# Kernel tuning notes

Hardware: AMD Instinct MI355X
Metric: run time of the kernel (lower is better)

Reference implementation:

```python
import jax, jax.numpy as jnp
import numpy as np

B = 2048      # env batch (graphs)
A = 8         # agents per graph (fully connected)
N = B * A     # total nodes
DIN = 192     # raw obs dim
HD = 256      # h_dim (base MLP)
MD = 256      # mem_dim (GRU)
GD = 128      # gnn_dim (per-head GATv2 out, concat=False -> head mean)
H = 4         # GAT heads
NA = 20       # n_actions
ED = 3        # edge_dim


def setup_inputs() -> dict:
    key = jax.random.key(0)
    ks = jax.random.split(key, 16)
    # fully-connected directed graph per group of A agents, no self loops
    s, d = np.meshgrid(np.arange(A), np.arange(A), indexing='ij')
    mask = s != d
    s = s[mask]; d = d[mask]                     # [A*(A-1)]
    off = (np.arange(B) * A)[:, None]
    src = (off + s[None, :]).reshape(-1)
    dst = (off + d[None, :]).reshape(-1)
    edge_index = jnp.asarray(np.stack([src, dst]), dtype=jnp.int32)  # [2, E]
    E = src.shape[0]
    p = lambda k, sh: jax.random.normal(ks[k], sh, jnp.float32) * 0.02
    return {
        'inputs': jax.random.normal(ks[0], (N, DIN), jnp.float32),
        'hidden_states': jax.random.normal(ks[1], (N, MD), jnp.float32) * 0.1,
        'edge_index': edge_index,
        'edge_attr': jax.random.uniform(ks[2], (E, ED), jnp.float32),
        # base MLP (2 layers: Linear+ReLU+LayerNorm)
        'W1': p(3, (DIN, HD)), 'b1': jnp.zeros(HD), 'g1': jnp.ones(HD), 'be1': jnp.zeros(HD),
        'W2': p(4, (HD, HD)),  'b2': jnp.zeros(HD), 'g2': jnp.ones(HD), 'be2': jnp.zeros(HD),
        # GRUCell
        'Wih': p(5, (3 * MD, HD)), 'Whh': p(6, (3 * MD, MD)),
        'bih': jnp.zeros(3 * MD), 'bhh': jnp.zeros(3 * MD),
        # GATv2Conv (edge_dim=3, heads=4, concat=False, residual)
        'Wl': p(7, (MD, H * GD)), 'bl': jnp.zeros(H * GD),
        'Wr': p(8, (MD, H * GD)), 'br': jnp.zeros(H * GD),
        'att': p(9, (H, GD)),
        'We': p(10, (ED, H * GD)),
        'Wres': p(11, (MD, GD)),
        'bg': jnp.zeros(GD),
        # head: LayerNorm + Linear
        'lng': jnp.ones(GD), 'lnb': jnp.zeros(GD),
        'Wout': p(12, (GD, NA)), 'bout': jnp.zeros(NA),
    }


def _ln(x, g, b):
    mu = jnp.mean(x, -1, keepdims=True)
    xc = x - mu
    v = jnp.mean(xc * xc, -1, keepdims=True)
    return xc * jax.lax.rsqrt(v + 1e-5) * g + b


def _fwd(inputs, hidden_states, edge_attr, edge_index,
         W1, b1, g1, be1, W2, b2, g2, be2,
         Wih, Whh, bih, bhh,
         Wl, bl, Wr, br, att, We, Wres, bg,
         lng, lnb, Wout, bout):
    src, dst = edge_index[0], edge_index[1]
    # ---- base MLP encode ----
    x = _ln(jax.nn.relu(inputs @ W1 + b1), g1, be1)
    x = _ln(jax.nn.relu(x @ W2 + b2), g2, be2)          # [N, HD]
    # ---- SimpleConv(aggr='mean', combine_root='self_loop') ----
    s = jax.ops.segment_sum(x[src], dst, num_segments=N) + x
    deg = jax.ops.segment_sum(jnp.ones(src.shape[0], x.dtype), dst, num_segments=N) + 1.0
    x = s / deg[:, None]                                 # [N, HD]
    # ---- GRUCell ----
    gi = x @ Wih.T + bih
    gh = hidden_states @ Whh.T + bhh
    ir, iz, inn = jnp.split(gi, 3, -1)
    hr, hz, hn = jnp.split(gh, 3, -1)
    r = jax.nn.sigmoid(ir + hr)
    z = jax.nn.sigmoid(iz + hz)
    n = jnp.tanh(inn + r * hn)
    h = (1.0 - z) * n + z * hidden_states                # [N, MD]
    # ---- GATv2Conv (add self loops, edge_attr fill='mean') ----
    loop = jnp.arange(N, dtype=src.dtype)
    sf = jnp.concatenate([src, loop])
    df = jnp.concatenate([dst, loop])
    ea = jnp.concatenate([edge_attr, jnp.broadcast_to(edge_attr.mean(0), (N, ED))], 0)
    xl = (h @ Wl + bl).reshape(N, H, GD)
    xr = (h @ Wr + br).reshape(N, H, GD)
    m = xl[sf] + xr[df] + (ea @ We).reshape(-1, H, GD)   # [Ef, H, GD]
    m = jnp.where(m > 0, m, 0.2 * m)                     # leaky_relu(0.2)
    logits = jnp.einsum('ehc,hc->eh', m, att)            # [Ef, H]
    mx = jax.ops.segment_max(logits, df, num_segments=N)
    ex = jnp.exp(logits - mx[df])
    den = jax.ops.segment_sum(ex, df, num_segments=N)
    alpha = ex / (den[df] + 1e-16)                       # segment softmax
    out = jax.ops.segment_sum(xl[sf] * alpha[..., None], df, num_segments=N)
    out = out.mean(1) + h @ Wres + bg                    # head mean + residual + bias
    zg = jax.nn.relu(out)                                # [N, GD]
    # ---- action head ----
    q = _ln(zg, lng, lnb) @ Wout + bout                  # [N, NA]
    return q, h


def reference(inputs, hidden_states, edge_index, edge_attr,
              W1, b1, g1, be1, W2, b2, g2, be2,
              Wih, Whh, bih, bhh,
              Wl, bl, Wr, br, att, We, Wres, bg,
              lng, lnb, Wout, bout):
    return _fwd(inputs, hidden_states, edge_attr, edge_index,
                W1, b1, g1, be1, W2, b2, g2, be2,
                Wih, Whh, bih, bhh,
                Wl, bl, Wr, br, att, We, Wres, bg,
                lng, lnb, Wout, bout)
```

## Files before the change

kernel.cpp:

```cpp
#include <hip/hip_runtime.h>
#include <hip/hip_bf16.h>

constexpr int NB  = 2048;
constexpr int AG  = 8;
constexpr int NN  = NB * AG;
constexpr int DIN = 192;
constexpr int HD  = 256;
constexpr int MD  = 256;
constexpr int GD  = 128;
constexpr int NA  = 20;
constexpr int NE  = NB * AG * (AG - 1);

typedef __attribute__((ext_vector_type(8))) short bfrag8;
typedef __attribute__((ext_vector_type(4))) short sfrag4;
typedef __attribute__((ext_vector_type(4))) float f32x4;

#define MFMA16(a, b, c) __builtin_amdgcn_mfma_f32_16x16x32_bf16((a), (b), (c), 0, 0, 0)

__device__ __forceinline__ float bf2f(__hip_bfloat16 x) { return __bfloat162float(x); }
__device__ __forceinline__ __hip_bfloat16 f2bf(float x) { return __float2bfloat16(x); }
__device__ __forceinline__ short f2bs(float x) {
    __hip_bfloat16 b = __float2bfloat16(x);
    return *reinterpret_cast<short*>(&b);
}
__device__ __forceinline__ bfrag8 ldf(const __hip_bfloat16* p) { return *(const bfrag8*)p; }
__device__ __forceinline__ bfrag8 ldf32(const float* p) {
    const f32x4 a = *(const f32x4*)p;
    const f32x4 b = *(const f32x4*)(p + 4);
    bfrag8 r;
    r[0] = f2bs(a[0]); r[1] = f2bs(a[1]); r[2] = f2bs(a[2]); r[3] = f2bs(a[3]);
    r[4] = f2bs(b[0]); r[5] = f2bs(b[1]); r[6] = f2bs(b[2]); r[7] = f2bs(b[3]);
    return r;
}
__device__ __forceinline__ float sigmf(float x) { return 1.f / (1.f + __expf(-x)); }
__device__ __forceinline__ float blo(unsigned u) { return __uint_as_float(u << 16); }
__device__ __forceinline__ float bhi(unsigned u) { return __uint_as_float(u & 0xffff0000u); }

__global__ __launch_bounds__(256) void k_prep(
    const float* __restrict__ W1, const float* __restrict__ W2,
    const float* __restrict__ Wih, const float* __restrict__ Whh,
    const float* __restrict__ Wl, const float* __restrict__ bl,
    const float* __restrict__ Wr, const float* __restrict__ br,
    const float* __restrict__ Wres, const float* __restrict__ Wout,
    const float* __restrict__ ea,
    __hip_bfloat16* __restrict__ W1T, __hip_bfloat16* __restrict__ W2T,
    __hip_bfloat16* __restrict__ WihB, __hip_bfloat16* __restrict__ WhhB,
    __hip_bfloat16* __restrict__ WcatT, float* __restrict__ WoutTf,
    float* __restrict__ bcat, float* __restrict__ ea_partials)
{
    __shared__ float sw[4][3];
    const int tid = threadIdx.x;
    if (blockIdx.x >= 3151) {
        const int b = blockIdx.x - 3151;
        float a0 = 0.f, a1 = 0.f, a2 = 0.f;
#pragma unroll
        for (int k = 0; k < 7; k++) {
            int e = b * 1792 + k * 256 + tid;
            a0 += ea[e * 3 + 0];
            a1 += ea[e * 3 + 1];
            a2 += ea[e * 3 + 2];
        }
#pragma unroll
        for (int off = 1; off < 64; off <<= 1) {
            a0 += __shfl_xor(a0, off); a1 += __shfl_xor(a1, off); a2 += __shfl_xor(a2, off);
        }
        if ((tid & 63) == 0) { sw[tid >> 6][0] = a0; sw[tid >> 6][1] = a1; sw[tid >> 6][2] = a2; }
        __syncthreads();
        if (tid == 0) {
            ea_partials[b * 3 + 0] = sw[0][0] + sw[1][0] + sw[2][0] + sw[3][0];
            ea_partials[b * 3 + 1] = sw[0][1] + sw[1][1] + sw[2][1] + sw[3][1];
            ea_partials[b * 3 + 2] = sw[0][2] + sw[1][2] + sw[2][2] + sw[3][2];
        }
        return;
    }
    int i = blockIdx.x * 256 + tid;
    if (i < 49152) { int o = i / 192, c = i % 192; W1T[i] = f2bf(W1[c * 256 + o]); return; }
    i -= 49152;
    if (i < 65536) { int o = i >> 8, c = i & 255; W2T[i] = f2bf(W2[c * 256 + o]); return; }
    i -= 65536;
    if (i < 196608) { WihB[i] = f2bf(Wih[i]); return; }
    i -= 196608;
    if (i < 196608) { WhhB[i] = f2bf(Whh[i]); return; }
    i -= 196608;
    if (i < 294912) {
        int o = i >> 8, c = i & 255;
        float v;
        if (o < 512)       v = Wl[c * 512 + o];
        else if (o < 1024) v = Wr[c * 512 + (o - 512)];
        else               v = Wres[c * 128 + (o - 1024)];
        WcatT[i] = f2bf(v); return;
    }
    i -= 294912;
    if (i < 2560) { int o = i >> 7, c = i & 127; WoutTf[i] = Wout[c * 20 + o]; return; }
    i -= 2560;
    if (i < 1152) {
        float v = 0.f;
        if (i < 512) v = bl[i]; else if (i < 1024) v = br[i - 512];
        bcat[i] = v;
    }
}

__global__ __launch_bounds__(256) void k_encode(
    const float* __restrict__ in,
    const __hip_bfloat16* __restrict__ W1T,
    const float* __restrict__ b1, const float* __restrict__ g1, const float* __restrict__ be1,
    const __hip_bfloat16* __restrict__ W2T,
    const float* __restrict__ b2, const float* __restrict__ g2, const float* __restrict__ be2,
    __hip_bfloat16* __restrict__ xm)
{
    __shared__ float sf[16][257];
    __shared__ alignas(16) __hip_bfloat16 sb[16][264];
    const int tid = threadIdx.x;
    const int lane = tid & 63, w = tid >> 6;
    const int r = lane & 15, q = lane >> 4;
    const int m0 = blockIdx.x * 16;

    {
        bfrag8 af[6];
        const float* ap = in + (size_t)(m0 + r) * DIN + q * 8;
#pragma unroll
        for (int kb = 0; kb < 6; kb++) af[kb] = ldf32(ap + kb * 32);
#pragma unroll
        for (int i = 0; i < 4; i++) {
            int t = w * 4 + i;
            const __hip_bfloat16* wp = W1T + (size_t)(t * 16 + r) * DIN + q * 8;
            bfrag8 bf[6];
#pragma unroll
            for (int kb = 0; kb < 6; kb++) bf[kb] = ldf(wp + kb * 32);
            f32x4 acc = (f32x4){0.f, 0.f, 0.f, 0.f};
#pragma unroll
            for (int kb = 0; kb < 6; kb++) acc = MFMA16(af[kb], bf[kb], acc);
            int col = t * 16 + r;
            float bias = b1[col];
#pragma unroll
            for (int reg = 0; reg < 4; reg++)
                sf[q * 4 + reg][col] = fmaxf(acc[reg] + bias, 0.f);
        }
    }
    __syncthreads();
    {
        int rowi = tid >> 4, c16 = tid & 15;
        float vals[16]; float s = 0.f, s2 = 0.f;
#pragma unroll
        for (int j = 0; j < 16; j++) { float v = sf[rowi][c16 + 16 * j]; vals[j] = v; s += v; s2 += v * v; }
#pragma unroll
        for (int off = 1; off < 16; off <<= 1) { s += __shfl_xor(s, off); s2 += __shfl_xor(s2, off); }
        float mean = s * (1.f / HD);
        float var = fmaxf(s2 * (1.f / HD) - mean * mean, 0.f);
        float rs = rsqrtf(var + 1e-5f);
#pragma unroll
        for (int j = 0; j < 16; j++) {
            int col = c16 + 16 * j;
            sb[rowi][col] = f2bf((vals[j] - mean) * rs * g1[col] + be1[col]);
        }
    }
    __syncthreads();

    {
        bfrag8 af[8];
        const __hip_bfloat16* ap = &sb[r][0];
#pragma unroll
        for (int kb = 0; kb < 8; kb++) af[kb] = ldf(ap + kb * 32 + q * 8);
        float outv[4][4];
#pragma unroll
        for (int i = 0; i < 4; i++) {
            int t = w * 4 + i;
            const __hip_bfloat16* wp = W2T + (size_t)(t * 16 + r) * HD + q * 8;
            bfrag8 bf[8];
#pragma unroll
            for (int kb = 0; kb < 8; kb++) bf[kb] = ldf(wp + kb * 32);
            f32x4 acc = (f32x4){0.f, 0.f, 0.f, 0.f};
#pragma unroll
            for (int kb = 0; kb < 8; kb++) acc = MFMA16(af[kb], bf[kb], acc);
#pragma unroll
            for (int reg = 0; reg < 4; reg++) outv[i][reg] = acc[reg];
        }
        __syncthreads();
#pragma unroll
        for (int i = 0; i < 4; i++) {
            int col = (w * 4 + i) * 16 + r;
            float bias = b2[col];
#pragma unroll
            for (int reg = 0; reg < 4; reg++)
                sf[q * 4 + reg][col] = fmaxf(outv[i][reg] + bias, 0.f);
        }
    }
    __syncthreads();
    {
        int rowi = tid >> 4, c16 = tid & 15;
        float vals[16]; float s = 0.f, s2 = 0.f;
#pragma unroll
        for (int j = 0; j < 16; j++) { float v = sf[rowi][c16 + 16 * j]; vals[j] = v; s += v; s2 += v * v; }
#pragma unroll
        for (int off = 1; off < 16; off <<= 1) { s += __shfl_xor(s, off); s2 += __shfl_xor(s2, off); }
        float mean = s * (1.f / HD);
        float var = fmaxf(s2 * (1.f / HD) - mean * mean, 0.f);
        float rs = rsqrtf(var + 1e-5f);
#pragma unroll
        for (int j = 0; j < 16; j++) {
            int col = c16 + 16 * j;
            sb[rowi][col] = f2bf((vals[j] - mean) * rs * g2[col] + be2[col]);
        }
    }
    __syncthreads();
    {
        int col = tid;
        float a0 = 0.f, a1 = 0.f;
#pragma unroll
        for (int i = 0; i < 8; i++) { a0 += bf2f(sb[i][col]); a1 += bf2f(sb[8 + i][col]); }
        xm[(size_t)(2 * blockIdx.x) * HD + col] = f2bf(a0 * 0.125f);
        xm[(size_t)(2 * blockIdx.x + 1) * HD + col] = f2bf(a1 * 0.125f);
    }
}

__global__ __launch_bounds__(256, 2) void k_gruG(
    const float* __restrict__ hprev,
    const __hip_bfloat16* __restrict__ WhhB,
    const float* __restrict__ bhh,
    const __hip_bfloat16* __restrict__ xm,
    const __hip_bfloat16* __restrict__ WihB,
    const float* __restrict__ bih,
    float* __restrict__ hout)
{
    __shared__ alignas(16) float sgi[16][200];
    const int tid = threadIdx.x;
    const int lane = tid & 63, w = tid >> 6;
    const int r = lane & 15, q = lane >> 4;
    const int bswz = (blockIdx.x & 7) * 64 + (blockIdx.x >> 3);
    const int m0 = (bswz >> 2) * 128;
    const int cg = (bswz & 3) * 64;

    {
        const int g0 = m0 >> 3;
        bfrag8 axm[8];
        const __hip_bfloat16* ap = xm + (size_t)(g0 + r) * MD + q * 8;
#pragma unroll
        for (int kb = 0; kb < 8; kb++) axm[kb] = ldf(ap + kb * 32);
#pragma unroll
        for (int i = 0; i < 3; i++) {
            const int n = w * 3 + i;
            const int gate = n >> 2, nj = n & 3;
            const int colG = gate * 256 + cg + nj * 16 + r;
            const __hip_bfloat16* wp = WihB + (size_t)colG * MD + q * 8;
            bfrag8 bf[8];
#pragma unroll
            for (int kb = 0; kb < 8; kb++) bf[kb] = ldf(wp + kb * 32);
            f32x4 acg = (f32x4){0.f, 0.f, 0.f, 0.f};
#pragma unroll
            for (int kb = 0; kb < 8; kb++) acg = MFMA16(axm[kb], bf[kb], acg);
            const float bias = bih[colG];
#pragma unroll
            for (int reg = 0; reg < 4; reg++)
                sgi[q * 4 + reg][n * 16 + r] = acg[reg] + bias;
        }
    }

    bfrag8 afr[2][8];
#pragma unroll
    for (int t = 0; t < 2; t++) {
        const float* ap = hprev + (size_t)(m0 + (w * 2 + t) * 16 + r) * MD + q * 8;
#pragma unroll
        for (int kb = 0; kb < 8; kb++) afr[t][kb] = ldf32(ap + kb * 32);
    }
    __syncthreads();

    f32x4 acc[2][12];
#pragma unroll
    for (int t = 0; t < 2; t++)
#pragma unroll
        for (int n = 0; n < 12; n++) acc[t][n] = (f32x4){0.f, 0.f, 0.f, 0.f};

#pragma unroll
    for (int kb = 0; kb < 8; kb++) {
        bfrag8 bfB[12];
#pragma unroll
        for (int g = 0; g < 3; g++)
#pragma unroll
            for (int nj = 0; nj < 4; nj++)
                bfB[g * 4 + nj] = ldf(WhhB + (size_t)(g * 256 + cg + nj * 16 + r) * MD
                                      + kb * 32 + q * 8);
#pragma unroll
        for (int t = 0; t < 2; t++)
#pragma unroll
            for (int n = 0; n < 12; n++)
                acc[t][n] = MFMA16(bfB[n], afr[t][kb], acc[t][n]);
    }

#pragma unroll
    for (int t = 0; t < 2; t++) {
        int node = m0 + (w * 2 + t) * 16 + r;
        int gl = ((w * 2 + t) * 16 + r) >> 3;
#pragma unroll
        for (int nj = 0; nj < 4; nj++) {
            int c = cg + nj * 16 + q * 4;
            int ci = nj * 16 + q * 4;
            f32x4 gR = *(const f32x4*)&sgi[gl][ci];
            f32x4 gZ = *(const f32x4*)&sgi[gl][64 + ci];
            f32x4 gN = *(const f32x4*)&sgi[gl][128 + ci];
            f32x4 bR = *(const f32x4*)&bhh[c];
            f32x4 bZ = *(const f32x4*)&bhh[256 + c];
            f32x4 bN = *(const f32x4*)&bhh[512 + c];
            f32x4 hp = *(const f32x4*)&hprev[(size_t)node * MD + c];
            f32x4 hv;
#pragma unroll
            for (int reg = 0; reg < 4; reg++) {
                float rr = sigmf(gR[reg] + acc[t][0 + nj][reg] + bR[reg]);
                float zz = sigmf(gZ[reg] + acc[t][4 + nj][reg] + bZ[reg]);
                float nn = tanhf(gN[reg] + rr * (acc[t][8 + nj][reg] + bN[reg]));
                hv[reg] = (1.f - zz) * nn + zz * hp[reg];
            }
            *(f32x4*)&hout[(size_t)node * MD + c] = hv;
        }
    }
}

__global__ __launch_bounds__(256, 4) void k_gat(
    const float* __restrict__ h,
    const __hip_bfloat16* __restrict__ WcatT,
    const float* __restrict__ bcat,
    const float* __restrict__ ea,
    const float* __restrict__ ea_partials,
    const float* __restrict__ att,
    const float* __restrict__ We,
    const float* __restrict__ bg,
    const float* __restrict__ lng, const float* __restrict__ lnb,
    const float* __restrict__ WoutTf,
    const float* __restrict__ bout,
    float* __restrict__ qout)
{
    __shared__ alignas(16) char smem_raw[16 * 1160 * 2];
    __shared__ float slog[2][4][8][8];
    __shared__ float smean[4];
    __hip_bfloat16 (*sx)[1160] = (__hip_bfloat16 (*)[1160])smem_raw;
    float (*szg)[136] = (float (*)[136])smem_raw;
    const int tid = threadIdx.x;
    const int lane = tid & 63, w = tid >> 6;
    const int m0 = blockIdx.x * 16;

    if (tid < 3) {
        float s = 0.f;
        for (int i = 0; i < 64; i++) s += ea_partials[i * 3 + tid];
        smean[tid] = s * (1.f / NE);
    }

    const int r = lane & 15, q = lane >> 4;
    const int sL = lane & 7, dL = lane >> 3;
    const int gg = w >> 1;
    float e0 = 0.f, e1 = 0.f, e2 = 0.f;
    if (sL != dL) {
        int eidx = sL * 7 + dL - (dL > sL ? 1 : 0);
        const float* ep = ea + (size_t)((blockIdx.x * 2 + gg) * 56 + eidx) * 3;
        e0 = ep[0]; e1 = ep[1]; e2 = ep[2];
    }

    {
        bfrag8 af[8];
        const float* ap = h + (size_t)(m0 + r) * MD + q * 8;
#pragma unroll
        for (int kb = 0; kb < 8; kb++) af[kb] = ldf32(ap + kb * 32);
#pragma unroll
        for (int i = 0; i < 18; i++) {
            const int t = i * 4 + w;
            const __hip_bfloat16* wp = WcatT + (size_t)(t * 16 + r) * MD + q * 8;
            bfrag8 bf[8];
#pragma unroll
            for (int kb = 0; kb < 8; kb++) bf[kb] = ldf(wp + kb * 32);
            f32x4 acc = (f32x4){0.f, 0.f, 0.f, 0.f};
#pragma unroll
            for (int kb = 0; kb < 8; kb++) acc = MFMA16(af[kb], bf[kb], acc);
            const int col = t * 16 + r;
            const float bias = bcat[col];
#pragma unroll
            for (int reg = 0; reg < 4; reg++)
                sx[q * 4 + reg][col] = f2bf(acc[reg] + bias);
        }
    }
    __syncthreads();
    if (sL == dL) { e0 = smean[0]; e1 = smean[1]; e2 = smean[2]; }

    {
        const __hip_bfloat16* xlrow = &sx[gg * 8 + sL][0];
        const __hip_bfloat16* xrrow = &sx[gg * 8 + dL][512];
#pragma unroll
        for (int t = 0; t < 2; t++) {
            const int hh = (w & 1) * 2 + t;
            const int woff = __builtin_amdgcn_readfirstlane(hh * 128);
            const float* attp = att + woff;
            const float* w0p = We + woff;
            const float* w1p = We + 512 + woff;
            const float* w2p = We + 1024 + woff;
            const __hip_bfloat16* xlp = xlrow + hh * 128;
            const __hip_bfloat16* xrp = xrrow + hh * 128;
            float p0 = 0.f, p1 = 0.f;
#pragma unroll 4
            for (int cb = 0; cb < 16; cb++) {
                const uint4 uxl = *(const uint4*)&xlp[cb * 8];
                const uint4 uxr = *(const uint4*)&xrp[cb * 8];
                const f32x4 a0  = *(const f32x4*)&attp[cb * 8];
                const f32x4 a1  = *(const f32x4*)&attp[cb * 8 + 4];
                const f32x4 w00 = *(const f32x4*)&w0p[cb * 8];
                const f32x4 w01 = *(const f32x4*)&w0p[cb * 8 + 4];
                const f32x4 w10 = *(const f32x4*)&w1p[cb * 8];
                const f32x4 w11 = *(const f32x4*)&w1p[cb * 8 + 4];
                const f32x4 w20 = *(const f32x4*)&w2p[cb * 8];
                const f32x4 w21 = *(const f32x4*)&w2p[cb * 8 + 4];
                float mm;
#define CH1(XL, XR, WA, WB, WC, AT, ACC)                                          \
                mm = fmaf(e2, (WC), fmaf(e1, (WB), fmaf(e0, (WA), (XL)))) + (XR); \
                mm = fmaxf(mm, 0.2f * mm); ACC = fmaf(mm, (AT), ACC);
                CH1(blo(uxl.x), blo(uxr.x), w00[0], w10[0], w20[0], a0[0], p0)
                CH1(bhi(uxl.x), bhi(uxr.x), w00[1], w10[1], w20[1], a0[1], p1)
                CH1(blo(uxl.y), blo(uxr.y), w00[2], w10[2], w20[2], a0[2], p0)
                CH1(bhi(uxl.y), bhi(uxr.y), w00[3], w10[3], w20[3], a0[3], p1)
                CH1(blo(uxl.z), blo(uxr.z), w01[0], w11[0], w21[0], a1[0], p0)
                CH1(bhi(uxl.z), bhi(uxr.z), w01[1], w11[1], w21[1], a1[1], p1)
                CH1(blo(uxl.w), blo(uxr.w), w01[2], w11[2], w21[2], a1[2], p0)
                CH1(bhi(uxl.w), bhi(uxr.w), w01[3], w11[3], w21[3], a1[3], p1)
#undef CH1
            }
            float p = p0 + p1;
            float mx = fmaxf(p, __shfl_xor(p, 1));
            mx = fmaxf(mx, __shfl_xor(mx, 2));
            mx = fmaxf(mx, __shfl_xor(mx, 4));
            float exv = __expf(p - mx);
            float den = exv + __shfl_xor(exv, 1);
            den += __shfl_xor(den, 2);
            den += __shfl_xor(den, 4);
            ((float*)&slog[gg][hh][0][0])[lane] = exv / (den + 1e-16f);
        }
    }
    __syncthreads();

    {
        const int d16 = tid >> 4, cb = (tid & 15) * 8;
        const int ag = d16 >> 3, dd = d16 & 7;
        float out[8] = {0.f, 0.f, 0.f, 0.f, 0.f, 0.f, 0.f, 0.f};
#pragma unroll
        for (int hh = 0; hh < 4; hh++) {
#pragma unroll
            for (int s = 0; s < 8; s++) {
                const float al = slog[ag][hh][dd][s];
                const uint4 u = *(const uint4*)&sx[ag * 8 + s][hh * 128 + cb];
                out[0] = fmaf(al, blo(u.x), out[0]);
                out[1] = fmaf(al, bhi(u.x), out[1]);
                out[2] = fmaf(al, blo(u.y), out[2]);
                out[3] = fmaf(al, bhi(u.y), out[3]);
                out[4] = fmaf(al, blo(u.z), out[4]);
                out[5] = fmaf(al, bhi(u.z), out[5]);
                out[6] = fmaf(al, blo(u.w), out[6]);
                out[7] = fmaf(al, bhi(u.w), out[7]);
            }
        }
        const uint4 ur = *(const uint4*)&sx[d16][1024 + cb];
        const f32x4 bg0 = *(const f32x4*)&bg[cb];
        const f32x4 bg1 = *(const f32x4*)&bg[cb + 4];
        f32x4 ov0, ov1;
        ov0[0] = fmaxf(out[0] * 0.25f + blo(ur.x) + bg0[0], 0.f);
        ov0[1] = fmaxf(out[1] * 0.25f + bhi(ur.x) + bg0[1], 0.f);
        ov0[2] = fmaxf(out[2] * 0.25f + blo(ur.y) + bg0[2], 0.f);
        ov0[3] = fmaxf(out[3] * 0.25f + bhi(ur.y) + bg0[3], 0.f);
        ov1[0] = fmaxf(out[4] * 0.25f + blo(ur.z) + bg1[0], 0.f);
        ov1[1] = fmaxf(out[5] * 0.25f + bhi(ur.z) + bg1[1], 0.f);
        ov1[2] = fmaxf(out[6] * 0.25f + blo(ur.w) + bg1[2], 0.f);
        ov1[3] = fmaxf(out[7] * 0.25f + bhi(ur.w) + bg1[3], 0.f);
        __syncthreads();
        *(f32x4*)&szg[d16][cb]     = ov0;
        *(f32x4*)&szg[d16][cb + 4] = ov1;
    }
    __syncthreads();

    {
        int row = tid >> 4, j = tid & 15;
        float v[8]; float s = 0.f, s2 = 0.f;
#pragma unroll
        for (int cj = 0; cj < 8; cj++) { v[cj] = szg[row][j + 16 * cj]; s += v[cj]; s2 += v[cj] * v[cj]; }
#pragma unroll
        for (int off = 1; off < 16; off <<= 1) { s += __shfl_xor(s, off); s2 += __shfl_xor(s2, off); }
        float mean = s * (1.f / GD);
        float var = fmaxf(s2 * (1.f / GD) - mean * mean, 0.f);
        float rs = rsqrtf(var + 1e-5f);
#pragma unroll
        for (int cj = 0; cj < 8; cj++) {
            int c = j + 16 * cj;
            szg[row][c] = (v[cj] - mean) * rs * lng[c] + lnb[c];
        }
    }
    __syncthreads();

    {
        int row = tid >> 4, j = tid & 15;
        for (int jj = j; jj < NA; jj += 16) {
            float a = bout[jj];
            const float* wo = WoutTf + jj * 128;
#pragma unroll
            for (int c4 = 0; c4 < 32; c4++) {
                f32x4 z = *(const f32x4*)&szg[row][c4 * 4];
                const f32x4 wv = *(const f32x4*)&wo[c4 * 4];
                a = fmaf(z[0], wv[0], a); a = fmaf(z[1], wv[1], a);
                a = fmaf(z[2], wv[2], a); a = fmaf(z[3], wv[3], a);
            }
            qout[(size_t)(m0 + row) * NA + jj] = a;
        }
    }
}

extern "C" void kernel_launch(void* const* d_in, const int* in_sizes, int n_in,
                              void* d_out, int out_size, void* d_ws, size_t ws_size,
                              hipStream_t stream) {
    const float* inp   = (const float*)d_in[0];
    const float* hid   = (const float*)d_in[1];
    const float* eatt  = (const float*)d_in[3];
    const float* W1    = (const float*)d_in[4];
    const float* b1    = (const float*)d_in[5];
    const float* g1    = (const float*)d_in[6];
    const float* be1   = (const float*)d_in[7];
    const float* W2    = (const float*)d_in[8];
    const float* b2    = (const float*)d_in[9];
    const float* g2    = (const float*)d_in[10];
    const float* be2   = (const float*)d_in[11];
    const float* Wih   = (const float*)d_in[12];
    const float* Whh   = (const float*)d_in[13];
    const float* bih   = (const float*)d_in[14];
    const float* bhh   = (const float*)d_in[15];
    const float* Wl    = (const float*)d_in[16];
    const float* bl    = (const float*)d_in[17];
    const float* Wr    = (const float*)d_in[18];
    const float* br    = (const float*)d_in[19];
    const float* att   = (const float*)d_in[20];
    const float* We    = (const float*)d_in[21];
    const float* Wres  = (const float*)d_in[22];
    const float* bg    = (const float*)d_in[23];
    const float* lng   = (const float*)d_in[24];
    const float* lnb   = (const float*)d_in[25];
    const float* Wout  = (const float*)d_in[26];
    const float* bout  = (const float*)d_in[27];

    float* qout = (float*)d_out;
    float* hout = (float*)d_out + (size_t)NN * NA;

    char* ws = (char*)d_ws;
    float*           ea_partials = (float*)ws;
    __hip_bfloat16*  xm    = (__hip_bfloat16*)(ws + 2048);
    __hip_bfloat16*  W1T   = (__hip_bfloat16*)(ws + 7342080);
    __hip_bfloat16*  W2T   = (__hip_bfloat16*)(ws + 7440384);
    __hip_bfloat16*  WihB  = (__hip_bfloat16*)(ws + 7571456);
    __hip_bfloat16*  WhhB  = (__hip_bfloat16*)(ws + 7964672);
    __hip_bfloat16*  WcatT = (__hip_bfloat16*)(ws + 8357888);
    float*           bcat  = (float*)(ws + 8947712);
    float*           WoutTf= (float*)(ws + 8952320);

    k_prep<<<3215, 256, 0, stream>>>(W1, W2, Wih, Whh, Wl, bl, Wr, br, Wres, Wout, eatt,
                                     W1T, W2T, WihB, WhhB, WcatT, WoutTf, bcat, ea_partials);
    k_encode<<<NN / 16, 256, 0, stream>>>(inp, W1T, b1, g1, be1, W2T, b2, g2, be2, xm);
    k_gruG<<<512, 256, 0, stream>>>(hid, WhhB, bhh, xm, WihB, bih, hout);
    k_gat<<<NB / 2, 256, 0, stream>>>(hout, WcatT, bcat, eatt, ea_partials, att, We, bg,
                                      lng, lnb, WoutTf, bout, qout);
}
```

Measured before the change: 312.6 us.

## Fuse encoder, GRU and GAT into one per-graph-pair kernel

Merges the encoder MLP, the GRU cell and the GATv2/head kernels into a single kernel where each block handles 16 nodes (2 graphs). The pooled encoder output, the GRU input gates and the new hidden state stay in shared memory and never go through global memory, and two kernel launches are removed. The cost is that each block now runs all GEMMs against a 16-row tile. The Wih GEMM does 16-row MFMAs on only 2 useful rows, and Whh is reloaded per 16 nodes instead of per 128, which raises weight traffic and wasted MFMA work.

```diff
diff --git a/kernel.cpp b/kernel.cpp
--- a/kernel.cpp
+++ b/kernel.cpp
@@ -100,222 +100,17 @@
     }
 }
 
-__global__ __launch_bounds__(256) void k_encode(
+__global__ __launch_bounds__(256, 4) void k_fused(
     const float* __restrict__ in,
     const __hip_bfloat16* __restrict__ W1T,
     const float* __restrict__ b1, const float* __restrict__ g1, const float* __restrict__ be1,
     const __hip_bfloat16* __restrict__ W2T,
     const float* __restrict__ b2, const float* __restrict__ g2, const float* __restrict__ be2,
-    __hip_bfloat16* __restrict__ xm)
-{
-    __shared__ float sf[16][257];
-    __shared__ alignas(16) __hip_bfloat16 sb[16][264];
-    const int tid = threadIdx.x;
-    const int lane = tid & 63, w = tid >> 6;
-    const int r = lane & 15, q = lane >> 4;
-    const int m0 = blockIdx.x * 16;
-
-    {
-        bfrag8 af[6];
-        const float* ap = in + (size_t)(m0 + r) * DIN + q * 8;
-#pragma unroll
-        for (int kb = 0; kb < 6; kb++) af[kb] = ldf32(ap + kb * 32);
-#pragma unroll
-        for (int i = 0; i < 4; i++) {
-            int t = w * 4 + i;
-            const __hip_bfloat16* wp = W1T + (size_t)(t * 16 + r) * DIN + q * 8;
-            bfrag8 bf[6];
-#pragma unroll
-            for (int kb = 0; kb < 6; kb++) bf[kb] = ldf(wp + kb * 32);
-            f32x4 acc = (f32x4){0.f, 0.f, 0.f, 0.f};
-#pragma unroll
-            for (int kb = 0; kb < 6; kb++) acc = MFMA16(af[kb], bf[kb], acc);
-            int col = t * 16 + r;
-            float bias = b1[col];
-#pragma unroll
-            for (int reg = 0; reg < 4; reg++)
-                sf[q * 4 + reg][col] = fmaxf(acc[reg] + bias, 0.f);
-        }
-    }
-    __syncthreads();
-    {
-        int rowi = tid >> 4, c16 = tid & 15;
-        float vals[16]; float s = 0.f, s2 = 0.f;
-#pragma unroll
-        for (int j = 0; j < 16; j++) { float v = sf[rowi][c16 + 16 * j]; vals[j] = v; s += v; s2 += v * v; }
-#pragma unroll
-        for (int off = 1; off < 16; off <<= 1) { s += __shfl_xor(s, off); s2 += __shfl_xor(s2, off); }
-        float mean = s * (1.f / HD);
-        float var = fmaxf(s2 * (1.f / HD) - mean * mean, 0.f);
-        float rs = rsqrtf(var + 1e-5f);
-#pragma unroll
-        for (int j = 0; j < 16; j++) {
-            int col = c16 + 16 * j;
-            sb[rowi][col] = f2bf((vals[j] - mean) * rs * g1[col] + be1[col]);
-        }
-    }
-    __syncthreads();
-
-    {
-        bfrag8 af[8];
-        const __hip_bfloat16* ap = &sb[r][0];
-#pragma unroll
-        for (int kb = 0; kb < 8; kb++) af[kb] = ldf(ap + kb * 32 + q * 8);
-        float outv[4][4];
-#pragma unroll
-        for (int i = 0; i < 4; i++) {
-            int t = w * 4 + i;
-            const __hip_bfloat16* wp = W2T + (size_t)(t * 16 + r) * HD + q * 8;
-            bfrag8 bf[8];
-#pragma unroll
-            for (int kb = 0; kb < 8; kb++) bf[kb] = ldf(wp + kb * 32);
-            f32x4 acc = (f32x4){0.f, 0.f, 0.f, 0.f};
-#pragma unroll
-            for (int kb = 0; kb < 8; kb++) acc = MFMA16(af[kb], bf[kb], acc);
-#pragma unroll
-            for (int reg = 0; reg < 4; reg++) outv[i][reg] = acc[reg];
-        }
-        __syncthreads();
-#pragma unroll
-        for (int i = 0; i < 4; i++) {
-            int col = (w * 4 + i) * 16 + r;
-            float bias = b2[col];
-#pragma unroll
-            for (int reg = 0; reg < 4; reg++)
-                sf[q * 4 + reg][col] = fmaxf(outv[i][reg] + bias, 0.f);
-        }
-    }
-    __syncthreads();
-    {
-        int rowi = tid >> 4, c16 = tid & 15;
-        float vals[16]; float s = 0.f, s2 = 0.f;
-#pragma unroll
-        for (int j = 0; j < 16; j++) { float v = sf[rowi][c16 + 16 * j]; vals[j] = v; s += v; s2 += v * v; }
-#pragma unroll
-        for (int off = 1; off < 16; off <<= 1) { s += __shfl_xor(s, off); s2 += __shfl_xor(s2, off); }
-        float mean = s * (1.f / HD);
-        float var = fmaxf(s2 * (1.f / HD) - mean * mean, 0.f);
-        float rs = rsqrtf(var + 1e-5f);
-#pragma unroll
-        for (int j = 0; j < 16; j++) {
-            int col = c16 + 16 * j;
-            sb[rowi][col] = f2bf((vals[j] - mean) * rs * g2[col] + be2[col]);
-        }
-    }
-    __syncthreads();
-    {
-        int col = tid;
-        float a0 = 0.f, a1 = 0.f;
-#pragma unroll
-        for (int i = 0; i < 8; i++) { a0 += bf2f(sb[i][col]); a1 += bf2f(sb[8 + i][col]); }
-        xm[(size_t)(2 * blockIdx.x) * HD + col] = f2bf(a0 * 0.125f);
-        xm[(size_t)(2 * blockIdx.x + 1) * HD + col] = f2bf(a1 * 0.125f);
-    }
-}
-
-__global__ __launch_bounds__(256, 2) void k_gruG(
     const float* __restrict__ hprev,
     const __hip_bfloat16* __restrict__ WhhB,
     const float* __restrict__ bhh,
-    const __hip_bfloat16* __restrict__ xm,
     const __hip_bfloat16* __restrict__ WihB,
     const float* __restrict__ bih,
-    float* __restrict__ hout)
-{
-    __shared__ alignas(16) float sgi[16][200];
-    const int tid = threadIdx.x;
-    const int lane = tid & 63, w = tid >> 6;
-    const int r = lane & 15, q = lane >> 4;
-    const int bswz = (blockIdx.x & 7) * 64 + (blockIdx.x >> 3);
-    const int m0 = (bswz >> 2) * 128;
-    const int cg = (bswz & 3) * 64;
-
-    {
-        const int g0 = m0 >> 3;
-        bfrag8 axm[8];
-        const __hip_bfloat16* ap = xm + (size_t)(g0 + r) * MD + q * 8;
-#pragma unroll
-        for (int kb = 0; kb < 8; kb++) axm[kb] = ldf(ap + kb * 32);
-#pragma unroll
-        for (int i = 0; i < 3; i++) {
-            const int n = w * 3 + i;
-            const int gate = n >> 2, nj = n & 3;
-            const int colG = gate * 256 + cg + nj * 16 + r;
-            const __hip_bfloat16* wp = WihB + (size_t)colG * MD + q * 8;
-            bfrag8 bf[8];
-#pragma unroll
-            for (int kb = 0; kb < 8; kb++) bf[kb] = ldf(wp + kb * 32);
-            f32x4 acg = (f32x4){0.f, 0.f, 0.f, 0.f};
-#pragma unroll
-            for (int kb = 0; kb < 8; kb++) acg = MFMA16(axm[kb], bf[kb], acg);
-            const float bias = bih[colG];
-#pragma unroll
-            for (int reg = 0; reg < 4; reg++)
-                sgi[q * 4 + reg][n * 16 + r] = acg[reg] + bias;
-        }
-    }
-
-    bfrag8 afr[2][8];
-#pragma unroll
-    for (int t = 0; t < 2; t++) {
-        const float* ap = hprev + (size_t)(m0 + (w * 2 + t) * 16 + r) * MD + q * 8;
-#pragma unroll
-        for (int kb = 0; kb < 8; kb++) afr[t][kb] = ldf32(ap + kb * 32);
-    }
-    __syncthreads();
-
-    f32x4 acc[2][12];
-#pragma unroll
-    for (int t = 0; t < 2; t++)
-#pragma unroll
-        for (int n = 0; n < 12; n++) acc[t][n] = (f32x4){0.f, 0.f, 0.f, 0.f};
-
-#pragma unroll
-    for (int kb = 0; kb < 8; kb++) {
-        bfrag8 bfB[12];
-#pragma unroll
-        for (int g = 0; g < 3; g++)
-#pragma unroll
-            for (int nj = 0; nj < 4; nj++)
-                bfB[g * 4 + nj] = ldf(WhhB + (size_t)(g * 256 + cg + nj * 16 + r) * MD
-                                      + kb * 32 + q * 8);
-#pragma unroll
-        for (int t = 0; t < 2; t++)
-#pragma unroll
-            for (int n = 0; n < 12; n++)
-                acc[t][n] = MFMA16(bfB[n], afr[t][kb], acc[t][n]);
-    }
-
-#pragma unroll
-    for (int t = 0; t < 2; t++) {
-        int node = m0 + (w * 2 + t) * 16 + r;
-        int gl = ((w * 2 + t) * 16 + r) >> 3;
-#pragma unroll
-        for (int nj = 0; nj < 4; nj++) {
-            int c = cg + nj * 16 + q * 4;
-            int ci = nj * 16 + q * 4;
-            f32x4 gR = *(const f32x4*)&sgi[gl][ci];
-            f32x4 gZ = *(const f32x4*)&sgi[gl][64 + ci];
-            f32x4 gN = *(const f32x4*)&sgi[gl][128 + ci];
-            f32x4 bR = *(const f32x4*)&bhh[c];
-            f32x4 bZ = *(const f32x4*)&bhh[256 + c];
-            f32x4 bN = *(const f32x4*)&bhh[512 + c];
-            f32x4 hp = *(const f32x4*)&hprev[(size_t)node * MD + c];
-            f32x4 hv;
-#pragma unroll
-            for (int reg = 0; reg < 4; reg++) {
-                float rr = sigmf(gR[reg] + acc[t][0 + nj][reg] + bR[reg]);
-                float zz = sigmf(gZ[reg] + acc[t][4 + nj][reg] + bZ[reg]);
-                float nn = tanhf(gN[reg] + rr * (acc[t][8 + nj][reg] + bN[reg]));
-                hv[reg] = (1.f - zz) * nn + zz * hp[reg];
-            }
-            *(f32x4*)&hout[(size_t)node * MD + c] = hv;
-        }
-    }
-}
-
-__global__ __launch_bounds__(256, 4) void k_gat(
-    const float* __restrict__ h,
     const __hip_bfloat16* __restrict__ WcatT,
     const float* __restrict__ bcat,
     const float* __restrict__ ea,
@@ -326,15 +121,22 @@
     const float* __restrict__ lng, const float* __restrict__ lnb,
     const float* __restrict__ WoutTf,
     const float* __restrict__ bout,
-    float* __restrict__ qout)
+    float* __restrict__ qout,
+    float* __restrict__ hout)
 {
-    __shared__ alignas(16) char smem_raw[16 * 1160 * 2];
+    __shared__ alignas(16) char smem[16 * 1160 * 2];
     __shared__ float slog[2][4][8][8];
     __shared__ float smean[4];
-    __hip_bfloat16 (*sx)[1160] = (__hip_bfloat16 (*)[1160])smem_raw;
-    float (*szg)[136] = (float (*)[136])smem_raw;
+    float          (*sf)[257]  = (float (*)[257])smem;
+    __hip_bfloat16 (*sb)[264]  = (__hip_bfloat16 (*)[264])(smem + 16448);
+    __hip_bfloat16 (*smx)[264] = (__hip_bfloat16 (*)[264])smem;
+    float          (*sgi)[768] = (float (*)[768])(smem + 24896);
+    __hip_bfloat16 (*sx)[1160] = (__hip_bfloat16 (*)[1160])smem;
+    float          (*szg)[136] = (float (*)[136])smem;
+
     const int tid = threadIdx.x;
     const int lane = tid & 63, w = tid >> 6;
+    const int r = lane & 15, q = lane >> 4;
     const int m0 = blockIdx.x * 16;
 
     if (tid < 3) {
@@ -342,8 +144,6 @@
         for (int i = 0; i < 64; i++) s += ea_partials[i * 3 + tid];
         smean[tid] = s * (1.f / NE);
     }
-
-    const int r = lane & 15, q = lane >> 4;
     const int sL = lane & 7, dL = lane >> 3;
     const int gg = w >> 1;
     float e0 = 0.f, e1 = 0.f, e2 = 0.f;
@@ -354,10 +154,181 @@
     }
 
     {
+        bfrag8 af[6];
+        const float* ap = in + (size_t)(m0 + r) * DIN + q * 8;
+#pragma unroll
+        for (int kb = 0; kb < 6; kb++) af[kb] = ldf32(ap + kb * 32);
+#pragma unroll
+        for (int i = 0; i < 4; i++) {
+            int t = w * 4 + i;
+            const __hip_bfloat16* wp = W1T + (size_t)(t * 16 + r) * DIN + q * 8;
+            bfrag8 bf[6];
+#pragma unroll
+            for (int kb = 0; kb < 6; kb++) bf[kb] = ldf(wp + kb * 32);
+            f32x4 acc = (f32x4){0.f, 0.f, 0.f, 0.f};
+#pragma unroll
+            for (int kb = 0; kb < 6; kb++) acc = MFMA16(af[kb], bf[kb], acc);
+            int col = t * 16 + r;
+            float bias = b1[col];
+#pragma unroll
+            for (int reg = 0; reg < 4; reg++)
+                sf[q * 4 + reg][col] = fmaxf(acc[reg] + bias, 0.f);
+        }
+    }
+    __syncthreads();
+    {
+        int rowi = tid >> 4, c16 = tid & 15;
+        float vals[16]; float s = 0.f, s2 = 0.f;
+#pragma unroll
+        for (int j = 0; j < 16; j++) { float v = sf[rowi][c16 + 16 * j]; vals[j] = v; s += v; s2 += v * v; }
+#pragma unroll
+        for (int off = 1; off < 16; off <<= 1) { s += __shfl_xor(s, off); s2 += __shfl_xor(s2, off); }
+        float mean = s * (1.f / HD);
+        float var = fmaxf(s2 * (1.f / HD) - mean * mean, 0.f);
+        float rs = rsqrtf(var + 1e-5f);
+#pragma unroll
+        for (int j = 0; j < 16; j++) {
+            int col = c16 + 16 * j;
+            sb[rowi][col] = f2bf((vals[j] - mean) * rs * g1[col] + be1[col]);
+        }
+    }
+    __syncthreads();
+    {
         bfrag8 af[8];
-        const float* ap = h + (size_t)(m0 + r) * MD + q * 8;
-#pragma unroll
-        for (int kb = 0; kb < 8; kb++) af[kb] = ldf32(ap + kb * 32);
+        const __hip_bfloat16* ap = &sb[r][0];
+#pragma unroll
+        for (int kb = 0; kb < 8; kb++) af[kb] = ldf(ap + kb * 32 + q * 8);
+        float outv[4][4];
+#pragma unroll
+        for (int i = 0; i < 4; i++) {
+            int t = w * 4 + i;
+            const __hip_bfloat16* wp = W2T + (size_t)(t * 16 + r) * HD + q * 8;
+            bfrag8 bf[8];
+#pragma unroll
+            for (int kb = 0; kb < 8; kb++) bf[kb] = ldf(wp + kb * 32);
+            f32x4 acc = (f32x4){0.f, 0.f, 0.f, 0.f};
+#pragma unroll
+            for (int kb = 0; kb < 8; kb++) acc = MFMA16(af[kb], bf[kb], acc);
+#pragma unroll
+            for (int reg = 0; reg < 4; reg++) outv[i][reg] = acc[reg];
+        }
+        __syncthreads();
+#pragma unroll
+        for (int i = 0; i < 4; i++) {
+            int col = (w * 4 + i) * 16 + r;
+            float bias = b2[col];
+#pragma unroll
+            for (int reg = 0; reg < 4; reg++)
+                sf[q * 4 + reg][col] = fmaxf(outv[i][reg] + bias, 0.f);
+        }
+    }
+    __syncthreads();
+    {
+        int rowi = tid >> 4, c16 = tid & 15;
+        float vals[16]; float s = 0.f, s2 = 0.f;
+#pragma unroll
+        for (int j = 0; j < 16; j++) { float v = sf[rowi][c16 + 16 * j]; vals[j] = v; s += v; s2 += v * v; }
+#pragma unroll
+        for (int off = 1; off < 16; off <<= 1) { s += __shfl_xor(s, off); s2 += __shfl_xor(s2, off); }
+        float mean = s * (1.f / HD);
+        float var = fmaxf(s2 * (1.f / HD) - mean * mean, 0.f);
+        float rs = rsqrtf(var + 1e-5f);
+#pragma unroll
+        for (int j = 0; j < 16; j++) {
+            int col = c16 + 16 * j;
+            sb[rowi][col] = f2bf((vals[j] - mean) * rs * g2[col] + be2[col]);
+        }
+    }
+    __syncthreads();
+    {
+        int col = tid;
+        float a0 = 0.f, a1 = 0.f;
+#pragma unroll
+        for (int i = 0; i < 8; i++) { a0 += bf2f(sb[i][col]); a1 += bf2f(sb[8 + i][col]); }
+        smx[0][col] = f2bf(a0 * 0.125f);
+        smx[1][col] = f2bf(a1 * 0.125f);
+#pragma unroll
+        for (int rr = 2; rr < 16; rr++) smx[rr][col] = f2bf(0.f);
+    }
+    __syncthreads();
+
+    {
+        bfrag8 axm[8];
+#pragma unroll
+        for (int kb = 0; kb < 8; kb++) axm[kb] = ldf(&smx[r][kb * 32 + q * 8]);
+#pragma unroll
+        for (int i = 0; i < 12; i++) {
+            const int t = w * 12 + i;
+            const __hip_bfloat16* wp = WihB + (size_t)(t * 16 + r) * MD + q * 8;
+            bfrag8 bf[8];
+#pragma unroll
+            for (int kb = 0; kb < 8; kb++) bf[kb] = ldf(wp + kb * 32);
+            f32x4 acg = (f32x4){0.f, 0.f, 0.f, 0.f};
+#pragma unroll
+            for (int kb = 0; kb < 8; kb++) acg = MFMA16(axm[kb], bf[kb], acg);
+            if (q == 0) {
+                const int colG = t * 16 + r;
+                const float bias = bih[colG];
+                sgi[0][colG] = acg[0] + bias;
+                sgi[1][colG] = acg[1] + bias;
+            }
+        }
+    }
+    __syncthreads();
+
+    {
+        bfrag8 afr[8];
+        const float* ap = hprev + (size_t)(m0 + r) * MD + q * 8;
+#pragma unroll
+        for (int kb = 0; kb < 8; kb++) afr[kb] = ldf32(ap + kb * 32);
+        f32x4 acc[12];
+#pragma unroll
+        for (int n = 0; n < 12; n++) acc[n] = (f32x4){0.f, 0.f, 0.f, 0.f};
+#pragma unroll
+        for (int kb = 0; kb < 8; kb++) {
+            bfrag8 bfB[12];
+#pragma unroll
+            for (int g = 0; g < 3; g++)
+#pragma unroll
+                for (int nj = 0; nj < 4; nj++)
+                    bfB[g * 4 + nj] = ldf(WhhB + (size_t)(g * 256 + w * 64 + nj * 16 + r) * MD
+                                          + kb * 32 + q * 8);
+#pragma unroll
+            for (int n = 0; n < 12; n++)
+                acc[n] = MFMA16(bfB[n], afr[kb], acc[n]);
+        }
+        const int node = m0 + r;
+        const int gl = r >> 3;
+#pragma unroll
+        for (int nj = 0; nj < 4; nj++) {
+            const int c = w * 64 + nj * 16 + q * 4;
+            f32x4 gR = *(const f32x4*)&sgi[gl][c];
+            f32x4 gZ = *(const f32x4*)&sgi[gl][256 + c];
+            f32x4 gN = *(const f32x4*)&sgi[gl][512 + c];
+            f32x4 bR = *(const f32x4*)&bhh[c];
+            f32x4 bZ = *(const f32x4*)&bhh[256 + c];
+            f32x4 bN = *(const f32x4*)&bhh[512 + c];
+            f32x4 hp = *(const f32x4*)&hprev[(size_t)node * MD + c];
+            f32x4 hv; sfrag4 pk;
+#pragma unroll
+            for (int reg = 0; reg < 4; reg++) {
+                float rr = sigmf(gR[reg] + acc[0 + nj][reg] + bR[reg]);
+                float zz = sigmf(gZ[reg] + acc[4 + nj][reg] + bZ[reg]);
+                float nn = tanhf(gN[reg] + rr * (acc[8 + nj][reg] + bN[reg]));
+                hv[reg] = (1.f - zz) * nn + zz * hp[reg];
+                pk[reg] = f2bs(hv[reg]);
+            }
+            *(f32x4*)&hout[(size_t)node * MD + c] = hv;
+            *(sfrag4*)&sb[r][c] = pk;
+        }
+    }
+    __syncthreads();
+
+    {
+        bfrag8 af[8];
+#pragma unroll
+        for (int kb = 0; kb < 8; kb++) af[kb] = ldf(&sb[r][kb * 32 + q * 8]);
+        __syncthreads();
 #pragma unroll
         for (int i = 0; i < 18; i++) {
             const int t = i * 4 + w;
@@ -540,7 +511,6 @@
 
     char* ws = (char*)d_ws;
     float*           ea_partials = (float*)ws;
-    __hip_bfloat16*  xm    = (__hip_bfloat16*)(ws + 2048);
     __hip_bfloat16*  W1T   = (__hip_bfloat16*)(ws + 7342080);
     __hip_bfloat16*  W2T   = (__hip_bfloat16*)(ws + 7440384);
     __hip_bfloat16*  WihB  = (__hip_bfloat16*)(ws + 7571456);
@@ -551,8 +521,8 @@
 
     k_prep<<<3215, 256, 0, stream>>>(W1, W2, Wih, Whh, Wl, bl, Wr, br, Wres, Wout, eatt,
                                      W1T, W2T, WihB, WhhB, WcatT, WoutTf, bcat, ea_partials);
-    k_encode<<<NN / 16, 256, 0, stream>>>(inp, W1T, b1, g1, be1, W2T, b2, g2, be2, xm);
-    k_gruG<<<512, 256, 0, stream>>>(hid, WhhB, bhh, xm, WihB, bih, hout);
-    k_gat<<<NB / 2, 256, 0, stream>>>(hout, WcatT, bcat, eatt, ea_partials, att, We, bg,
-                                      lng, lnb, WoutTf, bout, qout);
+    k_fused<<<NB / 2, 256, 0, stream>>>(inp, W1T, b1, g1, be1, W2T, b2, g2, be2,
+                                        hid, WhhB, bhh, WihB, bih, WcatT, bcat,
+                                        eatt, ea_partials, att, We, bg, lng, lnb,
+                                        WoutTf, bout, qout, hout);
 }
```

New measurement: 357.3 us. 1.14x slower.
